# Kernel optimization log

Measured on AMD Instinct MI355X. Metric: run time of the kernel, lower is better.

## Reference

```python
import jax, jax.numpy as jnp
import numpy as np

N = 50000        # nodes
DEG = 32         # in-degree per node
E = N * DEG      # edges
T = 4            # towers
NODE = 128       # node_dim
OUT = 128        # out_dim
IN_T = NODE // T   # 32, divide_input tower slice
OUT_T = OUT // T   # 32
AVG_D_LOG = float(np.log(5.0))  # avg_d = {'log': log(4+1)}
EPS = 1e-5


def setup_inputs() -> dict:
    key = jax.random.key(0)
    ks = jax.random.split(key, 6)
    h = jax.random.normal(ks[0], (N, NODE), jnp.float32)
    src = jax.random.randint(ks[1], (E,), 0, N)
    # every node gets exactly DEG incoming edges (sorted dst)
    dst = jnp.repeat(jnp.arange(N), DEG)
    # per-tower pretrans MLP (1 layer): Linear(2*IN_T -> OUT_T)
    W_pre = jax.random.normal(ks[2], (T, 2 * IN_T, OUT_T), jnp.float32) * 0.05
    b_pre = jnp.zeros((T, OUT_T), jnp.float32)
    # per-tower posttrans MLP (1 layer): Linear(12*OUT_T + IN_T -> OUT_T)
    W_post = jax.random.normal(ks[3], (T, 12 * OUT_T + IN_T, OUT_T), jnp.float32) * 0.05
    b_post = jnp.zeros((T, OUT_T), jnp.float32)
    # mixing network: Linear(OUT -> OUT) + LeakyReLU
    W_mix = jax.random.normal(ks[4], (OUT, OUT), jnp.float32) * 0.05
    b_mix = jnp.zeros((OUT,), jnp.float32)
    return dict(h=h, src=src, dst=dst, W_pre=W_pre, b_pre=b_pre,
                W_post=W_post, b_post=b_post, W_mix=W_mix, b_mix=b_mix)


def _pna_forward(h, src, dst, W_pre, b_pre, W_post, b_post, W_mix, b_mix):
    ht = h.reshape(N, T, IN_T)                    # divide_input: tower slices
    z2 = jnp.concatenate([ht[src], ht[dst]], axis=-1)   # [E,T,2*IN_T] (src||dst)
    # pretrans: MLP(1 layer) then ReLU
    e = jax.nn.relu(jnp.einsum('etk,tko->eto', z2, W_pre) + b_pre)  # [E,T,OUT_T]

    deg = jax.ops.segment_sum(jnp.ones((E,), h.dtype), dst, num_segments=N)  # [N]
    deg_c = jnp.maximum(deg, 1.0)[:, None, None]
    seg = lambda x: jax.ops.segment_sum(x, dst, num_segments=N)
    mean = seg(e) / deg_c                          # [N,T,OUT_T]
    mean_sq = seg(e * e) / deg_c
    std = jnp.sqrt(jax.nn.relu(mean_sq - mean * mean) + EPS)
    mx = jax.ops.segment_max(e, dst, num_segments=N)
    mn = jax.ops.segment_min(e, dst, num_segments=N)
    agg = jnp.concatenate([mean, mx, mn, std], axis=-1)   # [N,T,4*OUT_T]

    # scalers: identity, amplification, attenuation (D = in-degree)
    sc = jnp.log(deg + 1.0) / AVG_D_LOG            # [N]
    amp = agg * sc[:, None, None]
    att = agg / jnp.maximum(sc, EPS)[:, None, None]
    h_agg = jnp.concatenate([agg, amp, att], axis=-1)     # [N,T,12*OUT_T]

    # posttrans: cat(h_tower, aggregated) -> MLP(1 layer) -> ReLU
    z = jnp.concatenate([ht, h_agg], axis=-1)      # [N,T,IN_T+12*OUT_T]
    hp = jax.nn.relu(jnp.einsum('ntk,tko->nto', z, W_post) + b_post)  # [N,T,OUT_T]
    h_cat = hp.reshape(N, OUT)

    h_out = jax.nn.leaky_relu(h_cat @ W_mix + b_mix, 0.01)
    return h + h_out                               # residual (node_dim == out_dim)


def reference(h, src, dst, W_pre, b_pre, W_post, b_post, W_mix, b_mix):
    return _pna_forward(h, src, dst, W_pre, b_pre, W_post, b_post, W_mix, b_mix)
```

## Files before the change

### kernel.cpp

```cpp
#include <hip/hip_runtime.h>
#include <hip/hip_bf16.h>
#include <hip/hip_fp16.h>
#include <math.h>

#define N_NODES 50000
#define DEG     32
#define NBF     16
#define EPSV    1e-5f

typedef __attribute__((ext_vector_type(8))) short short8;
typedef __attribute__((ext_vector_type(4))) float f32x4;
typedef __attribute__((ext_vector_type(2))) _Float16 h16x2;
typedef __attribute__((ext_vector_type(4))) unsigned int uint4v;

__device__ __forceinline__ unsigned int bfpack(float a, float b) {
    return (unsigned int)__bfloat16_as_ushort(__float2bfloat16(a)) |
           ((unsigned int)__bfloat16_as_ushort(__float2bfloat16(b)) << 16);
}

__global__ void k_prep(const float* __restrict__ W_post, const float* __restrict__ W_mix,
                       const float* __restrict__ W_pre,
                       __hip_bfloat16* __restrict__ WeffT, __hip_bfloat16* __restrict__ WmixT,
                       __hip_bfloat16* __restrict__ WpreT, float sc, float isc) {
    int i = blockIdx.x * 256 + threadIdx.x;
    if (i < 20480) {
        int k = i % 160, to = i / 160, o = to & 31, t = to >> 5;
        const float* Wt = W_post + t * 416 * 32;
        float v;
        if (k < 32) v = Wt[k * 32 + o];
        else {
            int g = k - 32;
            v = Wt[(32 + g) * 32 + o] + sc * Wt[(160 + g) * 32 + o] + isc * Wt[(288 + g) * 32 + o];
        }
        WeffT[i] = __float2bfloat16(v);
    } else if (i < 36864) {
        int j = i - 20480;
        int k = j & 127, o = j >> 7;
        WmixT[j] = __float2bfloat16(W_mix[k * 128 + o]);
    } else {
        int q = i - 36864;
        int k = q & 31, o = (q >> 5) & 31, p = q >> 10;
        int t = p >> 1, half = p & 1;
        WpreT[q] = __float2bfloat16(W_pre[t * 2048 + (half * 32 + k) * 32 + o]);
    }
}

__global__ __launch_bounds__(256) void k_proj(const float* __restrict__ h,
        const __hip_bfloat16* __restrict__ WpreT, const float* __restrict__ b_pre,
        _Float16* __restrict__ Pd, _Float16* __restrict__ Ps) {
    __shared__ __align__(16) __hip_bfloat16 sA[64][136];
    int tid = threadIdx.x, w = tid >> 6, lane = tid & 63;
    int nb = blockIdx.x * 64;

    int colc = (tid & 31) * 4, rowb = tid >> 5;
#pragma unroll
    for (int i = 0; i < 8; ++i) {
        int row = i * 8 + rowb, n = nb + row;
        unsigned int lo = 0, hi = 0;
        if (n < N_NODES) {
            float4 f = *(const float4*)(h + n * 128 + colc);
            lo = bfpack(f.x, f.y); hi = bfpack(f.z, f.w);
        }
        *(uint2*)(&sA[row][colc]) = make_uint2(lo, hi);
    }
    __syncthreads();
    int col = lane & 15, quad = lane >> 4, r0 = w * 16;
    short8 a[4];
#pragma unroll
    for (int t = 0; t < 4; ++t)
        a[t] = *(const short8*)(&sA[r0 + col][t * 32 + quad * 8]);
    __syncthreads();
    unsigned short* sOut = (unsigned short*)sA;

#pragma unroll
    for (int half = 0; half < 2; ++half) {
#pragma unroll
        for (int t = 0; t < 4; ++t) {
#pragma unroll
            for (int ct = 0; ct < 2; ++ct) {
                int p = t * 2 + half, o = ct * 16 + col;
                short8 b = *(const short8*)(WpreT + p * 1024 + o * 32 + quad * 8);
                f32x4 acc = {0.f, 0.f, 0.f, 0.f};
                acc = __builtin_amdgcn_mfma_f32_16x16x32_bf16(a[t], b, acc, 0, 0, 0);
                float bp = half ? b_pre[t * 32 + o] : 0.f;
#pragma unroll
                for (int r = 0; r < 4; ++r)
                    sOut[(r0 + quad * 4 + r) * 136 + t * 32 + o] =
                        __half_as_ushort(__float2half(acc[r] + bp));
            }
        }
        __syncthreads();
        _Float16* dst = half ? Pd : Ps;
#pragma unroll
        for (int rr = 0; rr < 4; ++rr) {
            int chunk = rr * 256 + tid;
            int row = chunk >> 4, seg = chunk & 15, n = nb + row;
            if (n < N_NODES)
                *(uint4v*)(dst + n * 128 + seg * 8) =
                    *(const uint4v*)(&sOut[row * 136 + seg * 8]);
        }
        __syncthreads();
    }
}

__global__ __launch_bounds__(256) void k_fused(const float* __restrict__ h,
        const int* __restrict__ src, const _Float16* __restrict__ Pd,
        const _Float16* __restrict__ Ps, const __hip_bfloat16* __restrict__ WeffT,
        const __hip_bfloat16* __restrict__ WmixT, const float* __restrict__ b_post,
        const float* __restrict__ b_mix, float* __restrict__ out) {
    __shared__ __align__(16) __hip_bfloat16 sZ[NBF][648];
    __shared__ __align__(16) __hip_bfloat16 sHp[NBF][136];
    int tid = threadIdx.x, w = tid >> 6, lane = tid & 63;
    int nb = blockIdx.x * NBF;

    int lid = lane & 31, hsel = lane & 32;
    int cq = lid * 4;
    int tA = cq >> 5, oA = cq & 31;
    const h16x2 zeroh = {(_Float16)0.f, (_Float16)0.f};
    const h16x2 bigh  = {(_Float16)65504.f, (_Float16)65504.f};
#pragma unroll
    for (int it = 0; it < 2; ++it) {
        int row = it * 8 + w + (hsel >> 3);
        int n = nb + row;
        int vsrc = src[n * DEG + lid];
        float4 hv = *(const float4*)(h + n * 128 + cq);
        uint2 pdu = *(const uint2*)(Pd + n * 128 + cq);
        h16x2 pd01 = __builtin_bit_cast(h16x2, pdu.x);
        h16x2 pd23 = __builtin_bit_cast(h16x2, pdu.y);
        h16x2 sum01 = zeroh, sum23 = zeroh, sq01 = zeroh, sq23 = zeroh;
        h16x2 mx01 = zeroh, mx23 = zeroh;
        h16x2 mn01 = bigh, mn23 = bigh;
#pragma unroll
        for (int j0 = 0; j0 < DEG; j0 += 16) {
            uint2 pv[16];
#pragma unroll
            for (int u = 0; u < 16; ++u) {
                int s = __shfl(vsrc, (j0 + u) | hsel);
                pv[u] = *(const uint2*)(Ps + s * 128 + cq);
            }
#pragma unroll
            for (int u = 0; u < 16; ++u) {
                h16x2 f01 = __builtin_bit_cast(h16x2, pv[u].x);
                h16x2 f23 = __builtin_bit_cast(h16x2, pv[u].y);
                h16x2 e01 = __builtin_elementwise_max(f01 + pd01, zeroh);
                h16x2 e23 = __builtin_elementwise_max(f23 + pd23, zeroh);
                sum01 += e01; sq01 = e01 * e01 + sq01;
                mx01 = __builtin_elementwise_max(mx01, e01);
                mn01 = __builtin_elementwise_min(mn01, e01);
                sum23 += e23; sq23 = e23 * e23 + sq23;
                mx23 = __builtin_elementwise_max(mx23, e23);
                mn23 = __builtin_elementwise_min(mn23, e23);
            }
        }
        float mean0 = (float)sum01.x * (1.f / DEG), mean1 = (float)sum01.y * (1.f / DEG);
        float mean2 = (float)sum23.x * (1.f / DEG), mean3 = (float)sum23.y * (1.f / DEG);
        float sd0 = sqrtf(fmaxf((float)sq01.x * (1.f / DEG) - mean0 * mean0, 0.f) + EPSV);
        float sd1 = sqrtf(fmaxf((float)sq01.y * (1.f / DEG) - mean1 * mean1, 0.f) + EPSV);
        float sd2 = sqrtf(fmaxf((float)sq23.x * (1.f / DEG) - mean2 * mean2, 0.f) + EPSV);
        float sd3 = sqrtf(fmaxf((float)sq23.y * (1.f / DEG) - mean3 * mean3, 0.f) + EPSV);
        unsigned int* zr = (unsigned int*)(&sZ[row][tA * 160 + oA]);
        zr[0]  = bfpack(hv.x, hv.y);               zr[1]  = bfpack(hv.z, hv.w);
        zr[16] = bfpack(mean0, mean1);             zr[17] = bfpack(mean2, mean3);
        zr[32] = bfpack((float)mx01.x, (float)mx01.y);
        zr[33] = bfpack((float)mx23.x, (float)mx23.y);
        zr[48] = bfpack((float)mn01.x, (float)mn01.y);
        zr[49] = bfpack((float)mn23.x, (float)mn23.y);
        zr[64] = bfpack(sd0, sd1);                 zr[65] = bfpack(sd2, sd3);
    }
    __syncthreads();

    int col = lane & 15, quad = lane >> 4;
#pragma unroll
    for (int i = 0; i < 2; ++i) {
        int ct = w * 2 + i, t = ct >> 1, nt = ct & 1;
        f32x4 acc = {0.f, 0.f, 0.f, 0.f};
        int oc = t * 32 + nt * 16 + col;
        const __hip_bfloat16* wrow = WeffT + oc * 160 + quad * 8;
#pragma unroll
        for (int ks = 0; ks < 5; ++ks) {
            short8 a = *(const short8*)(&sZ[col][t * 160 + ks * 32 + quad * 8]);
            short8 b = *(const short8*)(wrow + ks * 32);
            acc = __builtin_amdgcn_mfma_f32_16x16x32_bf16(a, b, acc, 0, 0, 0);
        }
        float bp = b_post[oc];
#pragma unroll
        for (int r = 0; r < 4; ++r)
            sHp[quad * 4 + r][oc] = __float2bfloat16(fmaxf(acc[r] + bp, 0.f));
    }
    __syncthreads();

#pragma unroll
    for (int i = 0; i < 2; ++i) {
        int nt = w * 2 + i;
        f32x4 acc = {0.f, 0.f, 0.f, 0.f};
        int oc = nt * 16 + col;
        const __hip_bfloat16* wrow = WmixT + oc * 128 + quad * 8;
#pragma unroll
        for (int ks = 0; ks < 4; ++ks) {
            short8 a = *(const short8*)(&sHp[col][ks * 32 + quad * 8]);
            short8 b = *(const short8*)(wrow + ks * 32);
            acc = __builtin_amdgcn_mfma_f32_16x16x32_bf16(a, b, acc, 0, 0, 0);
        }
        float bm = b_mix[oc];
#pragma unroll
        for (int r = 0; r < 4; ++r) {
            int n = nb + quad * 4 + r;
            float m = acc[r] + bm;
            m = m > 0.f ? m : 0.01f * m;
            out[n * 128 + oc] = h[n * 128 + oc] + m;
        }
    }
}

extern "C" void kernel_launch(void* const* d_in, const int* in_sizes, int n_in,
                              void* d_out, int out_size, void* d_ws, size_t ws_size,
                              hipStream_t stream) {
    const float* h      = (const float*)d_in[0];
    const int*   src    = (const int*)d_in[1];
    const float* W_pre  = (const float*)d_in[3];
    const float* b_pre  = (const float*)d_in[4];
    const float* W_post = (const float*)d_in[5];
    const float* b_post = (const float*)d_in[6];
    const float* W_mix  = (const float*)d_in[7];
    const float* b_mix  = (const float*)d_in[8];
    float* out = (float*)d_out;

    char* ws = (char*)d_ws;
    __hip_bfloat16* WeffT = (__hip_bfloat16*)ws;
    __hip_bfloat16* WmixT = (__hip_bfloat16*)(ws + 40960);
    __hip_bfloat16* WpreT = (__hip_bfloat16*)(ws + 73728);
    _Float16*       Pd    = (_Float16*)(ws + 90112);
    _Float16*       Ps    = (_Float16*)(ws + 90112 + 12800000);

    double scd = log(33.0) / log(5.0);
    float sc = (float)scd, isc = (float)(1.0 / scd);

    hipLaunchKernelGGL(k_prep, dim3(176), dim3(256), 0, stream,
                       W_post, W_mix, W_pre, WeffT, WmixT, WpreT, sc, isc);
    hipLaunchKernelGGL(k_proj, dim3((N_NODES + 63) / 64), dim3(256), 0, stream,
                       h, WpreT, b_pre, Pd, Ps);
    hipLaunchKernelGGL(k_fused, dim3(N_NODES / NBF), dim3(256), 0, stream,
                       h, src, Pd, Ps, WeffT, WmixT, b_post, b_mix, out);
}
```

Measured before the change: 167.0 us.

## Replace MFMA bf16 projection with fp32 scalar per-node projection kernel

```diff
diff --git a/kernel.cpp b/kernel.cpp
--- a/kernel.cpp
+++ b/kernel.cpp
@@ -5,6 +5,7 @@
 
 #define N_NODES 50000
 #define DEG     32
+#define NBP     25
 #define NBF     16
 #define EPSV    1e-5f
 
@@ -19,9 +20,8 @@
 }
 
 __global__ void k_prep(const float* __restrict__ W_post, const float* __restrict__ W_mix,
-                       const float* __restrict__ W_pre,
                        __hip_bfloat16* __restrict__ WeffT, __hip_bfloat16* __restrict__ WmixT,
-                       __hip_bfloat16* __restrict__ WpreT, float sc, float isc) {
+                       float sc, float isc) {
     int i = blockIdx.x * 256 + threadIdx.x;
     if (i < 20480) {
         int k = i % 160, to = i / 160, o = to & 31, t = to >> 5;
@@ -33,73 +33,41 @@
             v = Wt[(32 + g) * 32 + o] + sc * Wt[(160 + g) * 32 + o] + isc * Wt[(288 + g) * 32 + o];
         }
         WeffT[i] = __float2bfloat16(v);
-    } else if (i < 36864) {
+    } else {
         int j = i - 20480;
         int k = j & 127, o = j >> 7;
         WmixT[j] = __float2bfloat16(W_mix[k * 128 + o]);
-    } else {
-        int q = i - 36864;
-        int k = q & 31, o = (q >> 5) & 31, p = q >> 10;
-        int t = p >> 1, half = p & 1;
-        WpreT[q] = __float2bfloat16(W_pre[t * 2048 + (half * 32 + k) * 32 + o]);
-    }
-}
-
-__global__ __launch_bounds__(256) void k_proj(const float* __restrict__ h,
-        const __hip_bfloat16* __restrict__ WpreT, const float* __restrict__ b_pre,
+    }
+}
+
+__global__ __launch_bounds__(128) void k_proj(const float* __restrict__ h,
+        const float* __restrict__ W_pre, const float* __restrict__ b_pre,
         _Float16* __restrict__ Pd, _Float16* __restrict__ Ps) {
-    __shared__ __align__(16) __hip_bfloat16 sA[64][136];
-    int tid = threadIdx.x, w = tid >> 6, lane = tid & 63;
-    int nb = blockIdx.x * 64;
-
-    int colc = (tid & 31) * 4, rowb = tid >> 5;
-#pragma unroll
-    for (int i = 0; i < 8; ++i) {
-        int row = i * 8 + rowb, n = nb + row;
-        unsigned int lo = 0, hi = 0;
-        if (n < N_NODES) {
-            float4 f = *(const float4*)(h + n * 128 + colc);
-            lo = bfpack(f.x, f.y); hi = bfpack(f.z, f.w);
-        }
-        *(uint2*)(&sA[row][colc]) = make_uint2(lo, hi);
-    }
-    __syncthreads();
-    int col = lane & 15, quad = lane >> 4, r0 = w * 16;
-    short8 a[4];
-#pragma unroll
-    for (int t = 0; t < 4; ++t)
-        a[t] = *(const short8*)(&sA[r0 + col][t * 32 + quad * 8]);
-    __syncthreads();
-    unsigned short* sOut = (unsigned short*)sA;
-
-#pragma unroll
-    for (int half = 0; half < 2; ++half) {
-#pragma unroll
-        for (int t = 0; t < 4; ++t) {
-#pragma unroll
-            for (int ct = 0; ct < 2; ++ct) {
-                int p = t * 2 + half, o = ct * 16 + col;
-                short8 b = *(const short8*)(WpreT + p * 1024 + o * 32 + quad * 8);
-                f32x4 acc = {0.f, 0.f, 0.f, 0.f};
-                acc = __builtin_amdgcn_mfma_f32_16x16x32_bf16(a[t], b, acc, 0, 0, 0);
-                float bp = half ? b_pre[t * 32 + o] : 0.f;
-#pragma unroll
-                for (int r = 0; r < 4; ++r)
-                    sOut[(r0 + quad * 4 + r) * 136 + t * 32 + o] =
-                        __half_as_ushort(__float2half(acc[r] + bp));
-            }
-        }
+    int c = threadIdx.x, t = c >> 5, o = c & 31;
+    const float* Wt = W_pre + t * 64 * 32;
+    float wsr[32], wdr[32];
+#pragma unroll
+    for (int k = 0; k < 32; ++k) { wsr[k] = Wt[k * 32 + o]; wdr[k] = Wt[(32 + k) * 32 + o]; }
+    float bp = b_pre[t * 32 + o];
+    __shared__ float sh[128];
+    int base = blockIdx.x * NBP;
+    for (int ni = 0; ni < NBP; ++ni) {
+        int n = base + ni;
         __syncthreads();
-        _Float16* dst = half ? Pd : Ps;
-#pragma unroll
-        for (int rr = 0; rr < 4; ++rr) {
-            int chunk = rr * 256 + tid;
-            int row = chunk >> 4, seg = chunk & 15, n = nb + row;
-            if (n < N_NODES)
-                *(uint4v*)(dst + n * 128 + seg * 8) =
-                    *(const uint4v*)(&sOut[row * 136 + seg * 8]);
-        }
+        sh[c] = h[n * 128 + c];
         __syncthreads();
+        const float4* h4 = (const float4*)(sh + t * 32);
+        float as = 0.f, ad = 0.f;
+#pragma unroll
+        for (int k4 = 0; k4 < 8; ++k4) {
+            float4 hv = h4[k4];
+            as = fmaf(hv.x, wsr[4*k4+0], as); ad = fmaf(hv.x, wdr[4*k4+0], ad);
+            as = fmaf(hv.y, wsr[4*k4+1], as); ad = fmaf(hv.y, wdr[4*k4+1], ad);
+            as = fmaf(hv.z, wsr[4*k4+2], as); ad = fmaf(hv.z, wdr[4*k4+2], ad);
+            as = fmaf(hv.w, wsr[4*k4+3], as); ad = fmaf(hv.w, wdr[4*k4+3], ad);
+        }
+        Ps[n * 128 + c] = (_Float16)as;
+        Pd[n * 128 + c] = (_Float16)(ad + bp);
     }
 }
 
@@ -228,17 +196,16 @@
     char* ws = (char*)d_ws;
     __hip_bfloat16* WeffT = (__hip_bfloat16*)ws;
     __hip_bfloat16* WmixT = (__hip_bfloat16*)(ws + 40960);
-    __hip_bfloat16* WpreT = (__hip_bfloat16*)(ws + 73728);
     _Float16*       Pd    = (_Float16*)(ws + 90112);
     _Float16*       Ps    = (_Float16*)(ws + 90112 + 12800000);
 
     double scd = log(33.0) / log(5.0);
     float sc = (float)scd, isc = (float)(1.0 / scd);
 
-    hipLaunchKernelGGL(k_prep, dim3(176), dim3(256), 0, stream,
-                       W_post, W_mix, W_pre, WeffT, WmixT, WpreT, sc, isc);
-    hipLaunchKernelGGL(k_proj, dim3((N_NODES + 63) / 64), dim3(256), 0, stream,
-                       h, WpreT, b_pre, Pd, Ps);
+    hipLaunchKernelGGL(k_prep, dim3(144), dim3(256), 0, stream,
+                       W_post, W_mix, WeffT, WmixT, sc, isc);
+    hipLaunchKernelGGL(k_proj, dim3(N_NODES / NBP), dim3(128), 0, stream,
+                       h, W_pre, b_pre, Pd, Ps);
     hipLaunchKernelGGL(k_fused, dim3(N_NODES / NBF), dim3(256), 0, stream,
                        h, src, Pd, Ps, WeffT, WmixT, b_post, b_mix, out);
 }
```

Result: slower. 180.7 us (+8.2%).
